# Kernel tuning notes

Hardware: AMD Instinct MI355X
Metric: run time of the kernel (lower is better)

Reference implementation:

```python
import jax, jax.numpy as jnp
import numpy as np

N, IN, OUT, E, S = 65536, 512, 512, 8, 64


def setup_inputs() -> dict:
    key = jax.random.key(0)
    k1, k2, k3, k4, k5 = jax.random.split(key, 5)
    bound = float(np.sqrt(1.0 / IN))
    x = jax.random.normal(k1, (N, IN), dtype=jnp.float32)
    expert_coefficients = jax.random.normal(k2, (S, E), dtype=jnp.float32)
    batch_indices = jax.random.randint(k3, (N,), 0, S)
    weights = jax.random.uniform(k4, (E, OUT, IN), dtype=jnp.float32, minval=-bound, maxval=bound)
    bias = jax.random.uniform(k5, (OUT,), dtype=jnp.float32, minval=-bound, maxval=bound)
    return {"x": x, "expert_coefficients": expert_coefficients,
            "batch_indices": batch_indices, "weights": weights, "bias": bias}


def reference(x, expert_coefficients, batch_indices, weights, bias):
    # Original computes mixed_weights[b] = sum_e coeff[b,e] * W[e], then for each
    # system b applies mixed_weights[b] to the atoms with batch_indices == b via a
    # masked scan. Linearity lets us equivalently gather per-atom expert
    # coefficients and contract once, avoiding the O(num_systems * N) waste:
    #   out[n,o] = sum_e coeff[batch_indices[n], e] * sum_i W[e,o,i] * x[n,i]
    coeff_per_atom = expert_coefficients[batch_indices]  # [N, E]
    out = jnp.einsum('ni,eoi,ne->no', x, weights, coeff_per_atom)  # [N, OUT]
    return out + bias
```

## Files before the change

### kernel.cpp

```cpp
#include <hip/hip_runtime.h>
#include <hip/hip_bf16.h>

#define NA   65536
#define DIN  512
#define DOUT 512
#define NE   8
#define NS   64
#define CAP  1280
#define BM   128
#define BN   128
#define BK   32
#define TPS  (CAP / BM)
#define NKT  (DIN / BK)
#define CSTR 32
#define TILE_US 4096

typedef __attribute__((ext_vector_type(8))) __bf16 bf16x8;
typedef __attribute__((ext_vector_type(4))) float floatx4;

__device__ __forceinline__ void async_load16(const void* g, void* l) {
  __builtin_amdgcn_global_load_lds(
      (__attribute__((address_space(1))) void*)(void*)g,
      (__attribute__((address_space(3))) void*)l,
      16, 0, 0);
}

__device__ __forceinline__ int b3(int c) { return c >= 3 ? c - 3 : c; }

__global__ void scatter_kernel(const int* __restrict__ bidx,
                               int* __restrict__ counts,
                               int* __restrict__ perm) {
  __shared__ int hist[NS];
  __shared__ int base[NS];
  int t = threadIdx.x;
  if (t < NS) hist[t] = 0;
  __syncthreads();
  int n = blockIdx.x * 256 + t;
  int s = bidx[n];
  int rank = atomicAdd(&hist[s], 1);
  __syncthreads();
  if (t < NS && hist[t] > 0) base[t] = atomicAdd(&counts[t * CSTR], hist[t]);
  __syncthreads();
  perm[s * CAP + base[s] + rank] = n;
}

__global__ void mixw_kernel(const float* __restrict__ W,
                            const float* __restrict__ coeff,
                            ushort* __restrict__ mixedW) {
  int t = threadIdx.x;
  int base = blockIdx.x * 2048 + t * 8;
  float w[NE][8];
#pragma unroll
  for (int e = 0; e < NE; e++) {
    const float4* p = (const float4*)(W + e * (DOUT * DIN) + base);
    float4 a = p[0], b = p[1];
    w[e][0] = a.x; w[e][1] = a.y; w[e][2] = a.z; w[e][3] = a.w;
    w[e][4] = b.x; w[e][5] = b.y; w[e][6] = b.z; w[e][7] = b.w;
  }
  int s0 = blockIdx.y * 8;
  for (int si = 0; si < 8; si++) {
    int s = s0 + si;
    float o[8] = {0, 0, 0, 0, 0, 0, 0, 0};
#pragma unroll
    for (int e = 0; e < NE; e++) {
      float c = coeff[s * NE + e];
#pragma unroll
      for (int j = 0; j < 8; j++) o[j] += c * w[e][j];
    }
    union { bf16x8 v; uint4 u; } cv;
#pragma unroll
    for (int j = 0; j < 8; j++) cv.v[j] = (__bf16)o[j];
    *(uint4*)(mixedW + (size_t)s * (DOUT * DIN) + base) = cv.u;
  }
}

__device__ __forceinline__ void gload_a(const float* g0, const float* g1,
                                        int kt, float4& s0, float4& s1,
                                        float4& s2, float4& s3) {
  const float* a0 = g0 + kt * BK;
  const float* a1 = g1 + kt * BK;
  s0 = *(const float4*)(a0);
  s1 = *(const float4*)(a0 + 4);
  s2 = *(const float4*)(a1);
  s3 = *(const float4*)(a1 + 4);
}

__device__ __forceinline__ void cvt_write(ushort* Ab, int wo0, int wo1,
                                          const float4& s0, const float4& s1,
                                          const float4& s2, const float4& s3) {
  bf16x8 h;
  h[0] = (__bf16)s0.x; h[1] = (__bf16)s0.y; h[2] = (__bf16)s0.z; h[3] = (__bf16)s0.w;
  h[4] = (__bf16)s1.x; h[5] = (__bf16)s1.y; h[6] = (__bf16)s1.z; h[7] = (__bf16)s1.w;
  *(bf16x8*)(Ab + wo0) = h;
  bf16x8 g;
  g[0] = (__bf16)s2.x; g[1] = (__bf16)s2.y; g[2] = (__bf16)s2.z; g[3] = (__bf16)s2.w;
  g[4] = (__bf16)s3.x; g[5] = (__bf16)s3.y; g[6] = (__bf16)s3.z; g[7] = (__bf16)s3.w;
  *(bf16x8*)(Ab + wo1) = g;
}

__global__ __launch_bounds__(256) void gemm_kernel(
    const float* __restrict__ x, const ushort* __restrict__ mixedW,
    const int* __restrict__ perm, const int* __restrict__ counts,
    const float* __restrict__ bias, float* __restrict__ out) {
  int nwg = gridDim.x * gridDim.y;
  int lin = blockIdx.y * gridDim.x + blockIdx.x;
  int cpx = nwg >> 3;
  int work = (lin & 7) * cpx + (lin >> 3);
  int bx = work & 3;
  int by = work >> 2;

  int s = by / TPS;
  int tt = by - s * TPS;
  int count = counts[s * CSTR];
  int r0 = tt * BM;
  if (r0 >= count) return;
  int rows = min(BM, count - r0);
  int n0 = bx * BN;

  __shared__ __align__(16) ushort Alds[3 * TILE_US];
  __shared__ __align__(16) ushort Blds[3 * TILE_US];
  __shared__ int prow[BM];

  int tid = threadIdx.x;
  int lane = tid & 63;
  int wave = tid >> 6;

  if (tid < BM) prow[tid] = perm[s * CAP + r0 + min(tid, rows - 1)];

  int chunk = lane & 3;
  int cxor = (lane >> 3) & 3;
  const float* agp0;
  const float* agp1;
  int awoff0, awoff1;
  {
    int rl0 = wave * 32 + (lane >> 2);
    int rl1 = rl0 + 16;
    int pr0 = perm[s * CAP + r0 + min(rl0, rows - 1)];
    int pr1 = perm[s * CAP + r0 + min(rl1, rows - 1)];
    agp0 = x + (size_t)pr0 * DIN + chunk * 8;
    agp1 = x + (size_t)pr1 * DIN + chunk * 8;
    int ac = chunk ^ cxor;
    awoff0 = rl0 * 32 + ac * 8;
    awoff1 = rl1 * 32 + ac * 8;
  }
  const ushort* bgp0;
  const ushort* bgp1;
  int boff0, boff1;
  {
    int bkc = (chunk ^ cxor) * 8;
    int row0 = (wave * 16) + (lane >> 2);
    int row1 = row0 + 64;
    bgp0 = mixedW + (size_t)s * (DOUT * DIN) + (size_t)(n0 + row0) * DIN + bkc;
    bgp1 = mixedW + (size_t)s * (DOUT * DIN) + (size_t)(n0 + row1) * DIN + bkc;
    boff0 = wave * 512;
    boff1 = (4 + wave) * 512;
  }

  floatx4 acc[4][4];
#pragma unroll
  for (int mt = 0; mt < 4; mt++)
#pragma unroll
    for (int nt = 0; nt < 4; nt++) acc[mt][nt] = {0.f, 0.f, 0.f, 0.f};

  int wm = wave >> 1, wn = wave & 1;
  int m15 = lane & 15, quad = lane >> 4;
  int rxor = (m15 >> 1) & 3;
  int rcol = (quad ^ rxor) * 8;
  int aro = (wm * 64 + m15) * 32 + rcol;
  int bro = (wn * 64 + m15) * 32 + rcol;

  float4 p0, p1, p2, p3, q0, q1, q2, q3;

  gload_a(agp0, agp1, 0, p0, p1, p2, p3);
  async_load16(bgp0, Blds + boff0);
  async_load16(bgp1, Blds + boff1);
  gload_a(agp0, agp1, 1, q0, q1, q2, q3);
  async_load16(bgp0 + BK, Blds + TILE_US + boff0);
  async_load16(bgp1 + BK, Blds + TILE_US + boff1);
  asm volatile("s_waitcnt vmcnt(8)" ::: "memory");
  cvt_write(Alds, awoff0, awoff1, p0, p1, p2, p3);

#define ITER(T, C0, C1, C2, C3, N0, N1, N2, N3)                        \
  {                                                                    \
    if ((T) + 2 < NKT) {                                               \
      int c2 = b3(c0 + 2);                                             \
      gload_a(agp0, agp1, (T) + 2, N0, N1, N2, N3);                    \
      async_load16(bgp0 + ((T) + 2) * BK, Blds + c2 * TILE_US + boff0);\
      async_load16(bgp1 + ((T) + 2) * BK, Blds + c2 * TILE_US + boff1);\
      asm volatile("s_waitcnt vmcnt(8)" ::: "memory");                 \
    } else if ((T) == NKT - 2) {                                       \
      asm volatile("s_waitcnt vmcnt(2)" ::: "memory");                 \
    } else {                                                           \
      asm volatile("s_waitcnt vmcnt(0)" ::: "memory");                 \
    }                                                                  \
    __builtin_amdgcn_s_barrier();                                      \
    __builtin_amdgcn_sched_barrier(0);                                 \
    if ((T) + 1 < NKT)                                                 \
      cvt_write(Alds + b3(c0 + 1) * TILE_US, awoff0, awoff1,           \
                C0, C1, C2, C3);                                       \
    {                                                                  \
      const ushort* Ab = Alds + c0 * TILE_US;                          \
      const ushort* Bb = Blds + c0 * TILE_US;                          \
      bf16x8 af[4], bfm[4];                                            \
      _Pragma("unroll")                                                \
      for (int i = 0; i < 4; i++) {                                    \
        af[i]  = *(const bf16x8*)(Ab + aro + i * 512);                 \
        bfm[i] = *(const bf16x8*)(Bb + bro + i * 512);                 \
      }                                                                \
      _Pragma("unroll")                                                \
      for (int mt = 0; mt < 4; mt++)                                   \
        _Pragma("unroll")                                              \
        for (int nt = 0; nt < 4; nt++)                                 \
          acc[mt][nt] = __builtin_amdgcn_mfma_f32_16x16x32_bf16(       \
              af[mt], bfm[nt], acc[mt][nt], 0, 0, 0);                  \
    }                                                                  \
    asm volatile("s_waitcnt lgkmcnt(0)" ::: "memory");                 \
    __builtin_amdgcn_sched_barrier(0);                                 \
    __builtin_amdgcn_s_barrier();                                      \
    c0 = b3(c0 + 1);                                                   \
  }

  int c0 = 0;
  for (int t = 0; t < NKT; t += 2) {
    ITER(t,     q0, q1, q2, q3, p0, p1, p2, p3);
    ITER(t + 1, p0, p1, p2, p3, q0, q1, q2, q3);
  }
#undef ITER

  float bv[4];
#pragma unroll
  for (int nt = 0; nt < 4; nt++) bv[nt] = bias[n0 + wn * 64 + nt * 16 + m15];

#pragma unroll
  for (int mt = 0; mt < 4; mt++) {
    int rb = wm * 64 + mt * 16 + quad * 4;
    int pr[4];
#pragma unroll
    for (int r = 0; r < 4; r++) pr[r] = prow[rb + r];
#pragma unroll
    for (int nt = 0; nt < 4; nt++) {
      int col = n0 + wn * 64 + nt * 16 + m15;
#pragma unroll
      for (int r = 0; r < 4; r++) {
        if (rb + r < rows)
          out[(size_t)pr[r] * DOUT + col] = acc[mt][nt][r] + bv[nt];
      }
    }
  }
}

extern "C" void kernel_launch(void* const* d_in, const int* in_sizes, int n_in,
                              void* d_out, int out_size, void* d_ws,
                              size_t ws_size, hipStream_t stream) {
  const float* x     = (const float*)d_in[0];
  const float* coeff = (const float*)d_in[1];
  const int*   bidx  = (const int*)d_in[2];
  const float* W     = (const float*)d_in[3];
  const float* bias  = (const float*)d_in[4];
  float* out = (float*)d_out;

  char* ws = (char*)d_ws;
  int* counts    = (int*)ws;
  int* perm      = (int*)(ws + NS * CSTR * 4);
  ushort* mixedW = (ushort*)(ws + NS * CSTR * 4 + NS * CAP * 4);

  hipMemsetAsync(counts, 0, NS * CSTR * sizeof(int), stream);
  hipLaunchKernelGGL(scatter_kernel, dim3(NA / 256), dim3(256), 0, stream,
                     bidx, counts, perm);
  hipLaunchKernelGGL(mixw_kernel, dim3(DOUT * DIN / 2048, 8), dim3(256), 0,
                     stream, W, coeff, mixedW);
  hipLaunchKernelGGL(gemm_kernel, dim3(DOUT / BN, NS * TPS), dim3(256), 0,
                     stream, x, mixedW, perm, counts, bias, out);
}
```

Baseline: 343.4 us.

## Merge prep kernels and deepen A-operand register prefetch to three stages

The scatter and mixed-weight kernels are merged into a single prep launch, with block index deciding the role. This removes one launch and lets the two independent jobs run concurrently. The GEMM main loop is also restructured into a fully unrolled loop with a three-slot register ring for the fp32 A tiles. The global load for tile t+3 is now issued after the MFMAs, and the bf16 convert and LDS write come after compute, so global latency has more cover. In exchange it uses more VGPRs for the extra float4 buffers and relies on the vmcnt waits still matching the new load ordering.

```diff
diff --git a/kernel.cpp b/kernel.cpp
--- a/kernel.cpp
+++ b/kernel.cpp
@@ -14,6 +14,7 @@
 #define NKT  (DIN / BK)
 #define CSTR 32
 #define TILE_US 4096
+#define NSCAT (NA / 256)
 
 typedef __attribute__((ext_vector_type(8))) __bf16 bf16x8;
 typedef __attribute__((ext_vector_type(4))) float floatx4;
@@ -25,76 +26,73 @@
       16, 0, 0);
 }
 
-__device__ __forceinline__ int b3(int c) { return c >= 3 ? c - 3 : c; }
-
-__global__ void scatter_kernel(const int* __restrict__ bidx,
-                               int* __restrict__ counts,
-                               int* __restrict__ perm) {
+__global__ void prep_kernel(const int* __restrict__ bidx,
+                            int* __restrict__ counts,
+                            int* __restrict__ perm,
+                            const float* __restrict__ W,
+                            const float* __restrict__ coeff,
+                            ushort* __restrict__ mixedW) {
   __shared__ int hist[NS];
   __shared__ int base[NS];
   int t = threadIdx.x;
-  if (t < NS) hist[t] = 0;
-  __syncthreads();
-  int n = blockIdx.x * 256 + t;
-  int s = bidx[n];
-  int rank = atomicAdd(&hist[s], 1);
-  __syncthreads();
-  if (t < NS && hist[t] > 0) base[t] = atomicAdd(&counts[t * CSTR], hist[t]);
-  __syncthreads();
-  perm[s * CAP + base[s] + rank] = n;
-}
-
-__global__ void mixw_kernel(const float* __restrict__ W,
-                            const float* __restrict__ coeff,
-                            ushort* __restrict__ mixedW) {
-  int t = threadIdx.x;
-  int base = blockIdx.x * 2048 + t * 8;
-  float w[NE][8];
-#pragma unroll
-  for (int e = 0; e < NE; e++) {
-    const float4* p = (const float4*)(W + e * (DOUT * DIN) + base);
-    float4 a = p[0], b = p[1];
-    w[e][0] = a.x; w[e][1] = a.y; w[e][2] = a.z; w[e][3] = a.w;
-    w[e][4] = b.x; w[e][5] = b.y; w[e][6] = b.z; w[e][7] = b.w;
-  }
-  int s0 = blockIdx.y * 8;
-  for (int si = 0; si < 8; si++) {
-    int s = s0 + si;
-    float o[8] = {0, 0, 0, 0, 0, 0, 0, 0};
+  if (blockIdx.x < NSCAT) {
+    if (t < NS) hist[t] = 0;
+    __syncthreads();
+    int n = blockIdx.x * 256 + t;
+    int s = bidx[n];
+    int rank = atomicAdd(&hist[s], 1);
+    __syncthreads();
+    if (t < NS && hist[t] > 0) base[t] = atomicAdd(&counts[t * CSTR], hist[t]);
+    __syncthreads();
+    perm[s * CAP + base[s] + rank] = n;
+  } else {
+    int bx = blockIdx.x - NSCAT;
+    int base_i = (bx & 127) * 2048 + t * 8;
+    float w[NE][8];
 #pragma unroll
     for (int e = 0; e < NE; e++) {
-      float c = coeff[s * NE + e];
-#pragma unroll
-      for (int j = 0; j < 8; j++) o[j] += c * w[e][j];
-    }
-    union { bf16x8 v; uint4 u; } cv;
-#pragma unroll
-    for (int j = 0; j < 8; j++) cv.v[j] = (__bf16)o[j];
-    *(uint4*)(mixedW + (size_t)s * (DOUT * DIN) + base) = cv.u;
+      const float4* p = (const float4*)(W + e * (DOUT * DIN) + base_i);
+      float4 a = p[0], b = p[1];
+      w[e][0] = a.x; w[e][1] = a.y; w[e][2] = a.z; w[e][3] = a.w;
+      w[e][4] = b.x; w[e][5] = b.y; w[e][6] = b.z; w[e][7] = b.w;
+    }
+    int s0 = (bx >> 7) * 8;
+    for (int si = 0; si < 8; si++) {
+      int s = s0 + si;
+      float o[8] = {0, 0, 0, 0, 0, 0, 0, 0};
+#pragma unroll
+      for (int e = 0; e < NE; e++) {
+        float c = coeff[s * NE + e];
+#pragma unroll
+        for (int j = 0; j < 8; j++) o[j] += c * w[e][j];
+      }
+      union { bf16x8 v; uint4 u; } cv;
+#pragma unroll
+      for (int j = 0; j < 8; j++) cv.v[j] = (__bf16)o[j];
+      *(uint4*)(mixedW + (size_t)s * (DOUT * DIN) + base_i) = cv.u;
+    }
   }
 }
 
 __device__ __forceinline__ void gload_a(const float* g0, const float* g1,
-                                        int kt, float4& s0, float4& s1,
-                                        float4& s2, float4& s3) {
+                                        int kt, float4* d) {
   const float* a0 = g0 + kt * BK;
   const float* a1 = g1 + kt * BK;
-  s0 = *(const float4*)(a0);
-  s1 = *(const float4*)(a0 + 4);
-  s2 = *(const float4*)(a1);
-  s3 = *(const float4*)(a1 + 4);
+  d[0] = *(const float4*)(a0);
+  d[1] = *(const float4*)(a0 + 4);
+  d[2] = *(const float4*)(a1);
+  d[3] = *(const float4*)(a1 + 4);
 }
 
 __device__ __forceinline__ void cvt_write(ushort* Ab, int wo0, int wo1,
-                                          const float4& s0, const float4& s1,
-                                          const float4& s2, const float4& s3) {
+                                          const float4* d) {
   bf16x8 h;
-  h[0] = (__bf16)s0.x; h[1] = (__bf16)s0.y; h[2] = (__bf16)s0.z; h[3] = (__bf16)s0.w;
-  h[4] = (__bf16)s1.x; h[5] = (__bf16)s1.y; h[6] = (__bf16)s1.z; h[7] = (__bf16)s1.w;
+  h[0] = (__bf16)d[0].x; h[1] = (__bf16)d[0].y; h[2] = (__bf16)d[0].z; h[3] = (__bf16)d[0].w;
+  h[4] = (__bf16)d[1].x; h[5] = (__bf16)d[1].y; h[6] = (__bf16)d[1].z; h[7] = (__bf16)d[1].w;
   *(bf16x8*)(Ab + wo0) = h;
   bf16x8 g;
-  g[0] = (__bf16)s2.x; g[1] = (__bf16)s2.y; g[2] = (__bf16)s2.z; g[3] = (__bf16)s2.w;
-  g[4] = (__bf16)s3.x; g[5] = (__bf16)s3.y; g[6] = (__bf16)s3.z; g[7] = (__bf16)s3.w;
+  g[0] = (__bf16)d[2].x; g[1] = (__bf16)d[2].y; g[2] = (__bf16)d[2].z; g[3] = (__bf16)d[2].w;
+  g[4] = (__bf16)d[3].x; g[5] = (__bf16)d[3].y; g[6] = (__bf16)d[3].z; g[7] = (__bf16)d[3].w;
   *(bf16x8*)(Ab + wo1) = g;
 }
 
@@ -169,63 +167,59 @@
   int aro = (wm * 64 + m15) * 32 + rcol;
   int bro = (wn * 64 + m15) * 32 + rcol;
 
-  float4 p0, p1, p2, p3, q0, q1, q2, q3;
-
-  gload_a(agp0, agp1, 0, p0, p1, p2, p3);
+  float4 As[3][4];
+
+  gload_a(agp0, agp1, 0, As[2]);
   async_load16(bgp0, Blds + boff0);
   async_load16(bgp1, Blds + boff1);
-  gload_a(agp0, agp1, 1, q0, q1, q2, q3);
+  gload_a(agp0, agp1, 1, As[0]);
   async_load16(bgp0 + BK, Blds + TILE_US + boff0);
   async_load16(bgp1 + BK, Blds + TILE_US + boff1);
-  asm volatile("s_waitcnt vmcnt(8)" ::: "memory");
-  cvt_write(Alds, awoff0, awoff1, p0, p1, p2, p3);
-
-#define ITER(T, C0, C1, C2, C3, N0, N1, N2, N3)                        \
-  {                                                                    \
-    if ((T) + 2 < NKT) {                                               \
-      int c2 = b3(c0 + 2);                                             \
-      gload_a(agp0, agp1, (T) + 2, N0, N1, N2, N3);                    \
-      async_load16(bgp0 + ((T) + 2) * BK, Blds + c2 * TILE_US + boff0);\
-      async_load16(bgp1 + ((T) + 2) * BK, Blds + c2 * TILE_US + boff1);\
-      asm volatile("s_waitcnt vmcnt(8)" ::: "memory");                 \
-    } else if ((T) == NKT - 2) {                                       \
-      asm volatile("s_waitcnt vmcnt(2)" ::: "memory");                 \
-    } else {                                                           \
-      asm volatile("s_waitcnt vmcnt(0)" ::: "memory");                 \
-    }                                                                  \
-    __builtin_amdgcn_s_barrier();                                      \
-    __builtin_amdgcn_sched_barrier(0);                                 \
-    if ((T) + 1 < NKT)                                                 \
-      cvt_write(Alds + b3(c0 + 1) * TILE_US, awoff0, awoff1,           \
-                C0, C1, C2, C3);                                       \
-    {                                                                  \
-      const ushort* Ab = Alds + c0 * TILE_US;                          \
-      const ushort* Bb = Blds + c0 * TILE_US;                          \
-      bf16x8 af[4], bfm[4];                                            \
-      _Pragma("unroll")                                                \
-      for (int i = 0; i < 4; i++) {                                    \
-        af[i]  = *(const bf16x8*)(Ab + aro + i * 512);                 \
-        bfm[i] = *(const bf16x8*)(Bb + bro + i * 512);                 \
-      }                                                                \
-      _Pragma("unroll")                                                \
-      for (int mt = 0; mt < 4; mt++)                                   \
-        _Pragma("unroll")                                              \
-        for (int nt = 0; nt < 4; nt++)                                 \
-          acc[mt][nt] = __builtin_amdgcn_mfma_f32_16x16x32_bf16(       \
-              af[mt], bfm[nt], acc[mt][nt], 0, 0, 0);                  \
-    }                                                                  \
-    asm volatile("s_waitcnt lgkmcnt(0)" ::: "memory");                 \
-    __builtin_amdgcn_sched_barrier(0);                                 \
-    __builtin_amdgcn_s_barrier();                                      \
-    c0 = b3(c0 + 1);                                                   \
-  }
-
-  int c0 = 0;
-  for (int t = 0; t < NKT; t += 2) {
-    ITER(t,     q0, q1, q2, q3, p0, p1, p2, p3);
-    ITER(t + 1, p0, p1, p2, p3, q0, q1, q2, q3);
-  }
-#undef ITER
+  gload_a(agp0, agp1, 2, As[1]);
+  asm volatile("s_waitcnt vmcnt(12)" ::: "memory");
+  cvt_write(Alds, awoff0, awoff1, As[2]);
+
+#pragma unroll
+  for (int t = 0; t < NKT; ++t) {
+    const int cb = t % 3;
+    const int wb = (t + 1) % 3;
+    const int nb = (t + 2) % 3;
+    if (t + 2 < NKT) {
+      async_load16(bgp0 + (t + 2) * BK, Blds + nb * TILE_US + boff0);
+      async_load16(bgp1 + (t + 2) * BK, Blds + nb * TILE_US + boff1);
+      asm volatile("s_waitcnt vmcnt(8)" ::: "memory");
+    } else if (t == NKT - 2) {
+      asm volatile("s_waitcnt vmcnt(2)" ::: "memory");
+    } else {
+      asm volatile("s_waitcnt vmcnt(0)" ::: "memory");
+    }
+    __builtin_amdgcn_s_barrier();
+    __builtin_amdgcn_sched_barrier(0);
+
+    {
+      const ushort* Ab = Alds + cb * TILE_US;
+      const ushort* Bb = Blds + cb * TILE_US;
+      bf16x8 af[4], bfm[4];
+#pragma unroll
+      for (int i = 0; i < 4; i++) {
+        af[i]  = *(const bf16x8*)(Ab + aro + i * 512);
+        bfm[i] = *(const bf16x8*)(Bb + bro + i * 512);
+      }
+#pragma unroll
+      for (int mt = 0; mt < 4; mt++)
+#pragma unroll
+        for (int nt = 0; nt < 4; nt++)
+          acc[mt][nt] = __builtin_amdgcn_mfma_f32_16x16x32_bf16(
+              af[mt], bfm[nt], acc[mt][nt], 0, 0, 0);
+    }
+    if (t + 1 < NKT)
+      cvt_write(Alds + wb * TILE_US, awoff0, awoff1, As[t % 3]);
+    if (t + 3 < NKT)
+      gload_a(agp0, agp1, t + 3, As[(t + 2) % 3]);
+    asm volatile("s_waitcnt lgkmcnt(0)" ::: "memory");
+    __builtin_amdgcn_sched_barrier(0);
+    __builtin_amdgcn_s_barrier();
+  }
 
   float bv[4];
 #pragma unroll
@@ -265,10 +259,8 @@
   ushort* mixedW = (ushort*)(ws + NS * CSTR * 4 + NS * CAP * 4);
 
   hipMemsetAsync(counts, 0, NS * CSTR * sizeof(int), stream);
-  hipLaunchKernelGGL(scatter_kernel, dim3(NA / 256), dim3(256), 0, stream,
-                     bidx, counts, perm);
-  hipLaunchKernelGGL(mixw_kernel, dim3(DOUT * DIN / 2048, 8), dim3(256), 0,
-                     stream, W, coeff, mixedW);
+  hipLaunchKernelGGL(prep_kernel, dim3(NSCAT + 128 * 8), dim3(256), 0, stream,
+                     bidx, counts, perm, W, coeff, mixedW);
   hipLaunchKernelGGL(gemm_kernel, dim3(DOUT / BN, NS * TPS), dim3(256), 0,
                      stream, x, mixedW, perm, counts, bias, out);
 }
```

Result: faster. 331.0 us (-3.6%).
